# Optimization experiments

Measured on AMD Instinct MI355X. Metric: run time of the kernel, lower is better.

## Reference

```python
import jax, jax.numpy as jnp
import numpy as np

N_NODE = 50000
N_EDGE = 625000
FDIM = 128
HID = 128
EPS = 1e-5


def setup_inputs() -> dict:
    key = jax.random.key(0)
    ks = jax.random.split(key, 12)
    node_feature = jax.random.normal(ks[0], (N_NODE, FDIM), dtype=jnp.float32)
    edge_matrix = jax.random.randint(ks[1], (2, N_EDGE), 0, N_NODE, dtype=jnp.int32)
    edge_feature = jax.random.normal(ks[2], (N_EDGE, FDIM), dtype=jnp.float32)
    in_dim = FDIM + FDIM  # concat(node, aggregated edge)
    s1 = 1.0 / np.sqrt(in_dim)
    s2 = 1.0 / np.sqrt(HID)
    W1 = jax.random.uniform(ks[3], (in_dim, HID), jnp.float32, -s1, s1)
    b1 = jax.random.uniform(ks[4], (HID,), jnp.float32, -s1, s1)
    W2 = jax.random.uniform(ks[5], (HID, HID), jnp.float32, -s2, s2)
    b2 = jax.random.uniform(ks[6], (HID,), jnp.float32, -s2, s2)
    W3 = jax.random.uniform(ks[7], (HID, FDIM), jnp.float32, -s2, s2)
    b3 = jax.random.uniform(ks[8], (FDIM,), jnp.float32, -s2, s2)
    gamma = jnp.ones((FDIM,), jnp.float32)
    beta = jnp.zeros((FDIM,), jnp.float32)
    return {"node_feature": node_feature, "edge_matrix": edge_matrix,
            "edge_feature": edge_feature, "W1": W1, "b1": b1, "W2": W2,
            "b2": b2, "W3": W3, "b3": b3, "gamma": gamma, "beta": beta}


def reference(node_feature, edge_matrix, edge_feature, W1, b1, W2, b2, W3, b3, gamma, beta):
    # receiver_idx = edge_matrix.T[:, 1] with edge_matrix [2, N_edge] -> row 1
    receiver_idx = edge_matrix[1]
    # scatter_add over receiver: [N_node, fdim]
    agg = jax.ops.segment_sum(edge_feature, receiver_idx, num_segments=node_feature.shape[0])
    x = jnp.concatenate([node_feature, agg], axis=-1)  # [N_node, 2*fdim]
    h = jax.nn.relu(x @ W1 + b1)
    h = jax.nn.relu(h @ W2 + b2)
    h = h @ W3 + b3
    # LayerNorm over last dim (eps = 1e-5, torch default)
    mu = jnp.mean(h, axis=-1, keepdims=True)
    var = jnp.mean((h - mu) ** 2, axis=-1, keepdims=True)
    h = (h - mu) * jax.lax.rsqrt(var + EPS) * gamma + beta
    return h + node_feature
```

## Files before the change

### kernel.cpp

```cpp
#include <hip/hip_runtime.h>
#include <hip/hip_bf16.h>

#define N_NODE 50000
#define N_EDGE 625000
#define FDIM 128
#define NB_SCAN 196

typedef __bf16 bf16x8 __attribute__((ext_vector_type(8)));
typedef float floatx4 __attribute__((ext_vector_type(4)));

#define MT 64
#define XS_LD 264
#define W_LD 40
#define H_LD 136

__global__ __launch_bounds__(256) void hist_kernel(
    const int* __restrict__ recv, int* __restrict__ count, int* __restrict__ pos)
{
    int e = blockIdx.x * 256 + threadIdx.x;
    if (e < N_EDGE) pos[e] = atomicAdd(&count[recv[e]], 1);
}

__global__ __launch_bounds__(256) void scan1_kernel(
    const int* __restrict__ count, int* __restrict__ off, int* __restrict__ bsum)
{
    __shared__ int s[256];
    int t = threadIdx.x;
    int i = blockIdx.x * 256 + t;
    int v = (i < N_NODE) ? count[i] : 0;
    s[t] = v;
    __syncthreads();
    for (int d = 1; d < 256; d <<= 1) {
        int x = (t >= d) ? s[t - d] : 0;
        __syncthreads();
        s[t] += x;
        __syncthreads();
    }
    if (i < N_NODE) off[i] = s[t] - v;
    if (t == 255) bsum[blockIdx.x] = s[255];
}

__global__ __launch_bounds__(256) void scan2_kernel(int* __restrict__ bsum)
{
    __shared__ int s[256];
    int t = threadIdx.x;
    int v = (t < NB_SCAN) ? bsum[t] : 0;
    s[t] = v;
    __syncthreads();
    for (int d = 1; d < 256; d <<= 1) {
        int x = (t >= d) ? s[t - d] : 0;
        __syncthreads();
        s[t] += x;
        __syncthreads();
    }
    if (t < NB_SCAN) bsum[t] = s[t] - v;
}

__global__ __launch_bounds__(256) void scan3_kernel(
    int* __restrict__ off, const int* __restrict__ bsum)
{
    int i = blockIdx.x * 256 + threadIdx.x;
    if (i < N_NODE) off[i] += bsum[blockIdx.x];
    if (i == N_NODE) off[i] = N_EDGE;
}

__global__ __launch_bounds__(256) void fill_kernel(
    const int* __restrict__ recv, const int* __restrict__ pos,
    const int* __restrict__ off, int* __restrict__ eid)
{
    int e = blockIdx.x * 256 + threadIdx.x;
    if (e < N_EDGE) {
        int r = recv[e];
        eid[off[r] + pos[e]] = e;
    }
}

__global__ __launch_bounds__(256, 2) void mlp_kernel(
    const float* __restrict__ nodef, const float* __restrict__ ef,
    const int* __restrict__ off, const int* __restrict__ eid,
    const float* __restrict__ W1, const float* __restrict__ b1,
    const float* __restrict__ W2, const float* __restrict__ b2,
    const float* __restrict__ W3, const float* __restrict__ b3,
    const float* __restrict__ gamma, const float* __restrict__ beta,
    float* __restrict__ out)
{
    __shared__ __bf16 xs[MT * XS_LD];
    __shared__ __bf16 wb[128 * W_LD];
    __shared__ __bf16 h1[MT * H_LD];
    __bf16* h2 = xs;

    const int t = threadIdx.x;
    const int wave = t >> 6;
    const int lane = t & 63;
    const int quad = lane >> 4;
    const int l16 = lane & 15;
    const int w16 = wave << 4;
    const int q8 = quad << 3;
    const int node0 = blockIdx.x * MT;

    const float4* nf4 = (const float4*)nodef;
#pragma unroll
    for (int i = 0; i < 8; ++i) {
        int it = i * 256 + t;
        int row = it >> 5;
        int c4 = it & 31;
        int node = node0 + row;
        if (node >= N_NODE) node = N_NODE - 1;
        float4 v = nf4[(long)node * 32 + c4];
        union { __bf16 b[4]; short4 s; } u;
        u.b[0] = (__bf16)v.x; u.b[1] = (__bf16)v.y;
        u.b[2] = (__bf16)v.z; u.b[3] = (__bf16)v.w;
        *(short4*)&xs[row * XS_LD + c4 * 4] = u.s;
    }

    const float2* ef2 = (const float2*)ef;
    for (int r0 = 0; r0 < 16; ++r0) {
        int row = w16 + r0;
        int node = node0 + row;
        float ax = 0.f, ay = 0.f;
        if (node < N_NODE) {
            int s0 = off[node], e0 = off[node + 1];
            int j = s0;
            for (; j + 4 <= e0; j += 4) {
                int i0 = eid[j], i1 = eid[j + 1], i2 = eid[j + 2], i3 = eid[j + 3];
                float2 v0 = ef2[(long)i0 * 64 + lane];
                float2 v1 = ef2[(long)i1 * 64 + lane];
                float2 v2 = ef2[(long)i2 * 64 + lane];
                float2 v3 = ef2[(long)i3 * 64 + lane];
                ax += v0.x + v1.x + v2.x + v3.x;
                ay += v0.y + v1.y + v2.y + v3.y;
            }
            for (; j < e0; ++j) {
                int i0 = eid[j];
                float2 v0 = ef2[(long)i0 * 64 + lane];
                ax += v0.x; ay += v0.y;
            }
        }
        union { __bf16 b[2]; int iv; } u;
        u.b[0] = (__bf16)ax; u.b[1] = (__bf16)ay;
        *(int*)&xs[row * XS_LD + 128 + lane * 2] = u.iv;
    }

    floatx4 acc[8];
    const floatx4 zero = {0.f, 0.f, 0.f, 0.f};

    auto stage_w = [&](const float* __restrict__ Wsrc, int k0) {
#pragma unroll
        for (int p = 0; p < 8; ++p) {
            int kl = p * 4 + ((t >> 7) << 1);
            int n = t & 127;
            float a0 = Wsrc[(k0 + kl) * 128 + n];
            float a1 = Wsrc[(k0 + kl + 1) * 128 + n];
            union { __bf16 b[2]; int i; } u;
            u.b[0] = (__bf16)a0; u.b[1] = (__bf16)a1;
            *(int*)&wb[n * W_LD + kl] = u.i;
        }
    };

    auto run_gemm = [&](const __bf16* A, int ldA, const float* __restrict__ Wsrc, int nk) {
#pragma unroll
        for (int nt = 0; nt < 8; ++nt) acc[nt] = zero;
        for (int kc = 0; kc < nk; ++kc) {
            stage_w(Wsrc, kc * 32);
            __syncthreads();
            bf16x8 a = *(const bf16x8*)&A[(w16 + l16) * ldA + kc * 32 + q8];
#pragma unroll
            for (int nt = 0; nt < 8; ++nt) {
                bf16x8 b = *(const bf16x8*)&wb[(nt * 16 + l16) * W_LD + q8];
                acc[nt] = __builtin_amdgcn_mfma_f32_16x16x32_bf16(a, b, acc[nt], 0, 0, 0);
            }
            __syncthreads();
        }
    };

    auto epilogue_relu = [&](const float* __restrict__ bias, __bf16* H) {
#pragma unroll
        for (int nt = 0; nt < 8; ++nt) {
            int col = nt * 16 + l16;
            float bv = bias[col];
#pragma unroll
            for (int r = 0; r < 4; ++r) {
                float v = acc[nt][r] + bv;
                v = v > 0.f ? v : 0.f;
                H[(w16 + quad * 4 + r) * H_LD + col] = (__bf16)v;
            }
        }
    };

    run_gemm(xs, XS_LD, W1, 8);
    epilogue_relu(b1, h1);
    run_gemm(h1, H_LD, W2, 4);
    epilogue_relu(b2, h2);
    run_gemm(h2, H_LD, W3, 4);

    float vout[8][4];
    float sum[4] = {0.f, 0.f, 0.f, 0.f};
    float sq[4]  = {0.f, 0.f, 0.f, 0.f};
#pragma unroll
    for (int nt = 0; nt < 8; ++nt) {
        int col = nt * 16 + l16;
        float bv = b3[col];
#pragma unroll
        for (int r = 0; r < 4; ++r) {
            float v = acc[nt][r] + bv;
            vout[nt][r] = v;
            sum[r] += v;
            sq[r] += v * v;
        }
    }
#pragma unroll
    for (int r = 0; r < 4; ++r) {
#pragma unroll
        for (int offs = 1; offs < 16; offs <<= 1) {
            sum[r] += __shfl_xor(sum[r], offs);
            sq[r]  += __shfl_xor(sq[r], offs);
        }
    }
    float mu[4], rs[4];
#pragma unroll
    for (int r = 0; r < 4; ++r) {
        mu[r] = sum[r] * (1.f / 128.f);
        float var = sq[r] * (1.f / 128.f) - mu[r] * mu[r];
        rs[r] = rsqrtf(var + 1e-5f);
    }
#pragma unroll
    for (int nt = 0; nt < 8; ++nt) {
        int col = nt * 16 + l16;
        float g = gamma[col], be = beta[col];
#pragma unroll
        for (int r = 0; r < 4; ++r) {
            int row = w16 + quad * 4 + r;
            int node = node0 + row;
            if (node < N_NODE) {
                long o = (long)node * 128 + col;
                out[o] = (vout[nt][r] - mu[r]) * rs[r] * g + be + nodef[o];
            }
        }
    }
}

extern "C" void kernel_launch(void* const* d_in, const int* in_sizes, int n_in,
                              void* d_out, int out_size, void* d_ws, size_t ws_size,
                              hipStream_t stream)
{
    const float* nodef = (const float*)d_in[0];
    const int*   em    = (const int*)d_in[1];
    const float* ef    = (const float*)d_in[2];
    const float* W1    = (const float*)d_in[3];
    const float* b1    = (const float*)d_in[4];
    const float* W2    = (const float*)d_in[5];
    const float* b2    = (const float*)d_in[6];
    const float* W3    = (const float*)d_in[7];
    const float* b3    = (const float*)d_in[8];
    const float* gamma = (const float*)d_in[9];
    const float* beta  = (const float*)d_in[10];
    float* out = (float*)d_out;

    int* count = (int*)d_ws;
    int* pos   = count + 50048;
    int* off   = pos + 625024;
    int* bsum  = off + 50048;
    int* eid   = bsum + 256;

    const int* recv = em + N_EDGE;

    hipMemsetAsync(count, 0, (size_t)N_NODE * sizeof(int), stream);

    int eblocks = (N_EDGE + 255) / 256;
    hist_kernel<<<eblocks, 256, 0, stream>>>(recv, count, pos);
    scan1_kernel<<<NB_SCAN, 256, 0, stream>>>(count, off, bsum);
    scan2_kernel<<<1, 256, 0, stream>>>(bsum);
    scan3_kernel<<<NB_SCAN, 256, 0, stream>>>(off, bsum);
    fill_kernel<<<eblocks, 256, 0, stream>>>(recv, pos, off, eid);

    int mblocks = (N_NODE + MT - 1) / MT;
    mlp_kernel<<<mblocks, 256, 0, stream>>>(nodef, ef, off, eid,
                                            W1, b1, W2, b2, W3, b3,
                                            gamma, beta, out);
}
```

Before: 630.8 us.

## Split edge gather into its own wave-per-node kernel and merge scan passes

Moves the per-node edge aggregation out of the MLP kernel into a separate gather kernel with one wave per node, so 12500 blocks expose far more memory-level parallelism than the 782 occupancy-limited MLP blocks did. Edge ids are loaded cooperatively once per 64-edge chunk and broadcast with shuffles. The aggregate is written as bf16 to a workspace buffer, which the MLP kernel reads with vectorised loads. The second and third scan kernels are merged so every block redoes the block-sum scan, saving one launch. The cost is an extra global round trip for the aggregate and one more kernel launch.

```diff
diff --git a/kernel.cpp b/kernel.cpp
--- a/kernel.cpp
+++ b/kernel.cpp
@@ -40,7 +40,8 @@
     if (t == 255) bsum[blockIdx.x] = s[255];
 }
 
-__global__ __launch_bounds__(256) void scan2_kernel(int* __restrict__ bsum)
+__global__ __launch_bounds__(256) void scan2_kernel(
+    int* __restrict__ off, const int* __restrict__ bsum)
 {
     __shared__ int s[256];
     int t = threadIdx.x;
@@ -53,14 +54,8 @@
         s[t] += x;
         __syncthreads();
     }
-    if (t < NB_SCAN) bsum[t] = s[t] - v;
-}
-
-__global__ __launch_bounds__(256) void scan3_kernel(
-    int* __restrict__ off, const int* __restrict__ bsum)
-{
-    int i = blockIdx.x * 256 + threadIdx.x;
-    if (i < N_NODE) off[i] += bsum[blockIdx.x];
+    int i = blockIdx.x * 256 + t;
+    if (i < N_NODE) off[i] += s[blockIdx.x] - ((blockIdx.x < NB_SCAN) ? bsum[blockIdx.x] : 0);
     if (i == N_NODE) off[i] = N_EDGE;
 }
 
@@ -75,9 +70,44 @@
     }
 }
 
+__global__ __launch_bounds__(256) void gather_kernel(
+    const float2* __restrict__ ef2, const int* __restrict__ off,
+    const int* __restrict__ eid, int* __restrict__ agg32)
+{
+    int wave = threadIdx.x >> 6;
+    int lane = threadIdx.x & 63;
+    int node = blockIdx.x * 4 + wave;
+    float ax = 0.f, ay = 0.f;
+    int s0 = off[node], e0 = off[node + 1];
+    for (int base = s0; base < e0; base += 64) {
+        int cnt = e0 - base; if (cnt > 64) cnt = 64;
+        int my_e = (lane < cnt) ? eid[base + lane] : 0;
+        int j = 0;
+        for (; j + 4 <= cnt; j += 4) {
+            int ea = __shfl(my_e, j);
+            int eb = __shfl(my_e, j + 1);
+            int ec = __shfl(my_e, j + 2);
+            int ed = __shfl(my_e, j + 3);
+            float2 va = ef2[(long)ea * 64 + lane];
+            float2 vb = ef2[(long)eb * 64 + lane];
+            float2 vc = ef2[(long)ec * 64 + lane];
+            float2 vd = ef2[(long)ed * 64 + lane];
+            ax += va.x + vb.x + vc.x + vd.x;
+            ay += va.y + vb.y + vc.y + vd.y;
+        }
+        for (; j < cnt; ++j) {
+            int e = __shfl(my_e, j);
+            float2 v = ef2[(long)e * 64 + lane];
+            ax += v.x; ay += v.y;
+        }
+    }
+    union { __bf16 b[2]; int iv; } u;
+    u.b[0] = (__bf16)ax; u.b[1] = (__bf16)ay;
+    agg32[(long)node * 64 + lane] = u.iv;
+}
+
 __global__ __launch_bounds__(256, 2) void mlp_kernel(
-    const float* __restrict__ nodef, const float* __restrict__ ef,
-    const int* __restrict__ off, const int* __restrict__ eid,
+    const float* __restrict__ nodef, const int* __restrict__ agg32,
     const float* __restrict__ W1, const float* __restrict__ b1,
     const float* __restrict__ W2, const float* __restrict__ b2,
     const float* __restrict__ W3, const float* __restrict__ b3,
@@ -112,33 +142,16 @@
         u.b[2] = (__bf16)v.z; u.b[3] = (__bf16)v.w;
         *(short4*)&xs[row * XS_LD + c4 * 4] = u.s;
     }
-
-    const float2* ef2 = (const float2*)ef;
-    for (int r0 = 0; r0 < 16; ++r0) {
-        int row = w16 + r0;
+    const int4* ag4 = (const int4*)agg32;
+#pragma unroll
+    for (int i = 0; i < 4; ++i) {
+        int it = i * 256 + t;
+        int row = it >> 4;
+        int c8 = it & 15;
         int node = node0 + row;
-        float ax = 0.f, ay = 0.f;
-        if (node < N_NODE) {
-            int s0 = off[node], e0 = off[node + 1];
-            int j = s0;
-            for (; j + 4 <= e0; j += 4) {
-                int i0 = eid[j], i1 = eid[j + 1], i2 = eid[j + 2], i3 = eid[j + 3];
-                float2 v0 = ef2[(long)i0 * 64 + lane];
-                float2 v1 = ef2[(long)i1 * 64 + lane];
-                float2 v2 = ef2[(long)i2 * 64 + lane];
-                float2 v3 = ef2[(long)i3 * 64 + lane];
-                ax += v0.x + v1.x + v2.x + v3.x;
-                ay += v0.y + v1.y + v2.y + v3.y;
-            }
-            for (; j < e0; ++j) {
-                int i0 = eid[j];
-                float2 v0 = ef2[(long)i0 * 64 + lane];
-                ax += v0.x; ay += v0.y;
-            }
-        }
-        union { __bf16 b[2]; int iv; } u;
-        u.b[0] = (__bf16)ax; u.b[1] = (__bf16)ay;
-        *(int*)&xs[row * XS_LD + 128 + lane * 2] = u.iv;
+        if (node >= N_NODE) node = N_NODE - 1;
+        int4 v = ag4[(long)node * 16 + c8];
+        *(int4*)&xs[row * XS_LD + 128 + c8 * 8] = v;
     }
 
     floatx4 acc[8];
@@ -261,6 +274,7 @@
     int* off   = pos + 625024;
     int* bsum  = off + 50048;
     int* eid   = bsum + 256;
+    int* agg32 = eid + 625024;
 
     const int* recv = em + N_EDGE;
 
@@ -269,12 +283,11 @@
     int eblocks = (N_EDGE + 255) / 256;
     hist_kernel<<<eblocks, 256, 0, stream>>>(recv, count, pos);
     scan1_kernel<<<NB_SCAN, 256, 0, stream>>>(count, off, bsum);
-    scan2_kernel<<<1, 256, 0, stream>>>(bsum);
-    scan3_kernel<<<NB_SCAN, 256, 0, stream>>>(off, bsum);
+    scan2_kernel<<<NB_SCAN, 256, 0, stream>>>(off, bsum);
     fill_kernel<<<eblocks, 256, 0, stream>>>(recv, pos, off, eid);
+    gather_kernel<<<N_NODE / 4, 256, 0, stream>>>((const float2*)ef, off, eid, agg32);
 
     int mblocks = (N_NODE + MT - 1) / MT;
-    mlp_kernel<<<mblocks, 256, 0, stream>>>(nodef, ef, off, eid,
-                                            W1, b1, W2, b2, W3, b3,
-                                            gamma, beta, out);
-}
+    mlp_kernel<<<mblocks, 256, 0, stream>>>(nodef, agg32, W1, b1, W2, b2,
+                                            W3, b3, gamma, beta, out);
+}
```

New measurement: 553.6 us. 1.14x faster.
